# Kernel optimization log

Measured on AMD Instinct MI355X. Metric: run time of the kernel, lower is better.

Reference implementation:

```python
import jax, jax.numpy as jnp
import numpy as np

DEPTH = 6; HEADS = 6; DIM = 384; HD = DIM // HEADS
WS = 14; WINDOW_BLOCKS = (0, 1, 3, 4)
IMG = 512; PATCH = 16; GRID = IMG // PATCH        # 32x32 token grid
PRE_GRID = 14                                      # 224 // 16 pretrain grid
SCALE = HD ** -0.5


def layer_norm(x, w, b, eps=1e-5):
    u = x.mean(-1, keepdims=True)
    s = ((x - u) ** 2).mean(-1, keepdims=True)
    return (x - u) / jnp.sqrt(s + eps) * w + b


def get_rel_pos(size, rel_pos):
    # q_size == k_size here; relative coords in [0, 2*size-2]
    coords = jnp.arange(size)[:, None] - jnp.arange(size)[None, :] + (size - 1)
    return rel_pos[coords]  # (size, size, HD)


def attention(x, qkv_w, qkv_b, proj_w, proj_b, rel_h, rel_w):
    B, H, W, C = x.shape
    N = H * W
    qkv = (x.reshape(B, N, C) @ qkv_w.T + qkv_b).reshape(B, N, 3, HEADS, HD)
    qkv = jnp.moveaxis(qkv, 2, 0).transpose(0, 1, 3, 2, 4)  # (3,B,h,N,d)
    q, k, v = qkv[0], qkv[1], qkv[2]
    attn = jnp.einsum('bhqd,bhkd->bhqk', q * SCALE, k)
    # decomposed relative position bias (ViTDet add_decomposed_rel_pos)
    Rh = get_rel_pos(H, rel_h)  # (H,H,d)
    Rw = get_rel_pos(W, rel_w)  # (W,W,d)
    rq = q.reshape(B, HEADS, H, W, HD)
    bias_h = jnp.einsum('bnhwc,hkc->bnhwk', rq, Rh)  # (B,h,H,W,H)
    bias_w = jnp.einsum('bnhwc,wkc->bnhwk', rq, Rw)  # (B,h,H,W,W)
    attn = (attn.reshape(B, HEADS, H, W, H, W)
            + bias_h[..., :, None] + bias_w[..., None, :]).reshape(B, HEADS, N, N)
    attn = jax.nn.softmax(attn, axis=-1)
    out = jnp.einsum('bhqk,bhkd->bhqd', attn, v)
    out = out.transpose(0, 2, 1, 3).reshape(B, H, W, C)
    return out @ proj_w.T + proj_b


def window_partition(x, ws):
    B, H, W, C = x.shape
    pad_h = (ws - H % ws) % ws
    pad_w = (ws - W % ws) % ws
    x = jnp.pad(x, ((0, 0), (0, pad_h), (0, pad_w), (0, 0)))
    Hp, Wp = H + pad_h, W + pad_w
    x = x.reshape(B, Hp // ws, ws, Wp // ws, ws, C)
    x = x.transpose(0, 1, 3, 2, 4, 5).reshape(-1, ws, ws, C)
    return x, Hp, Wp


def window_unpartition(win, ws, Hp, Wp, H, W):
    B = win.shape[0] // ((Hp // ws) * (Wp // ws))
    x = win.reshape(B, Hp // ws, Wp // ws, ws, ws, -1)
    x = x.transpose(0, 1, 3, 2, 4, 5).reshape(B, Hp, Wp, -1)
    return x[:, :H, :W]


def block(x, p, windowed):
    shortcut = x
    x = layer_norm(x, p['n1w'], p['n1b'])
    if windowed:
        H, W = x.shape[1], x.shape[2]
        x, Hp, Wp = window_partition(x, WS)
    x = attention(x, p['qw'], p['qb'], p['pw'], p['pb'], p['rh'], p['rw'])
    if windowed:
        x = window_unpartition(x, WS, Hp, Wp, H, W)
    x = shortcut + x
    h = layer_norm(x, p['n2w'], p['n2b'])
    h = jax.nn.gelu(h @ p['f1w'].T + p['f1b'], approximate=False)
    return x + h @ p['f2w'].T + p['f2b']


def vit_forward(x, patch_w, patch_b, pos_embed, norm1_w, norm1_b, qkv_w, qkv_b,
                proj_w, proj_b, norm2_w, norm2_b, fc1_w, fc1_b, fc2_w, fc2_b,
                rel_pos_h, rel_pos_w):
    y = jax.lax.conv_general_dilated(
        x, patch_w, (PATCH, PATCH), 'VALID',
        dimension_numbers=('NCHW', 'OIHW', 'NCHW'))
    y = y.transpose(0, 2, 3, 1) + patch_b  # (B, GRID, GRID, DIM)
    # abs pos embed: bicubic resize from pretrain 14x14 grid to 32x32
    pos = pos_embed.reshape(1, PRE_GRID, PRE_GRID, DIM)
    pos = jax.image.resize(pos, (1, GRID, GRID, DIM), 'bicubic')
    y = y + pos
    for i in range(DEPTH):
        windowed = i in WINDOW_BLOCKS
        L = 2 * WS - 1 if windowed else 2 * GRID - 1
        p = dict(n1w=norm1_w[i], n1b=norm1_b[i], qw=qkv_w[i], qb=qkv_b[i],
                 pw=proj_w[i], pb=proj_b[i], rh=rel_pos_h[i, :L], rw=rel_pos_w[i, :L],
                 n2w=norm2_w[i], n2b=norm2_b[i], f1w=fc1_w[i], f1b=fc1_b[i],
                 f2w=fc2_w[i], f2b=fc2_b[i])
        y = block(y, p, windowed)
    return y.transpose(0, 3, 1, 2)  # (B, DIM, GRID, GRID) 'last_feat'


def setup_inputs() -> dict:
    key = jax.random.key(0)
    ks = jax.random.split(key, 10)
    B = 4
    std = 0.02
    f32 = jnp.float32
    return {
        'x': jax.random.normal(ks[0], (B, 3, IMG, IMG), f32),
        'patch_w': jax.random.normal(ks[1], (DIM, 3, PATCH, PATCH), f32) * 0.05,
        'patch_b': jnp.zeros((DIM,), f32),
        'pos_embed': jax.random.normal(ks[2], (1, PRE_GRID * PRE_GRID, DIM), f32) * std,
        'norm1_w': jnp.ones((DEPTH, DIM), f32),
        'norm1_b': jnp.zeros((DEPTH, DIM), f32),
        'qkv_w': jax.random.normal(ks[3], (DEPTH, 3 * DIM, DIM), f32) * std,
        'qkv_b': jnp.zeros((DEPTH, 3 * DIM), f32),
        'proj_w': jax.random.normal(ks[4], (DEPTH, DIM, DIM), f32) * std,
        'proj_b': jnp.zeros((DEPTH, DIM), f32),
        'norm2_w': jnp.ones((DEPTH, DIM), f32),
        'norm2_b': jnp.zeros((DEPTH, DIM), f32),
        'fc1_w': jax.random.normal(ks[5], (DEPTH, 4 * DIM, DIM), f32) * std,
        'fc1_b': jnp.zeros((DEPTH, 4 * DIM), f32),
        'fc2_w': jax.random.normal(ks[6], (DEPTH, DIM, 4 * DIM), f32) * std,
        'fc2_b': jnp.zeros((DEPTH, DIM), f32),
        'rel_pos_h': jax.random.normal(ks[7], (DEPTH, 2 * GRID - 1, HD), f32) * std,
        'rel_pos_w': jax.random.normal(ks[8], (DEPTH, 2 * GRID - 1, HD), f32) * std,
    }


def reference(x, patch_w, patch_b, pos_embed, norm1_w, norm1_b, qkv_w, qkv_b,
              proj_w, proj_b, norm2_w, norm2_b, fc1_w, fc1_b, fc2_w, fc2_b,
              rel_pos_h, rel_pos_w):
    return vit_forward(x, patch_w, patch_b, pos_embed, norm1_w, norm1_b, qkv_w, qkv_b,
                       proj_w, proj_b, norm2_w, norm2_b, fc1_w, fc1_b, fc2_w, fc2_b,
                       rel_pos_h, rel_pos_w)
```

## Files before the change

kernel.cpp:

```cpp
#include <hip/hip_runtime.h>
#include <hip/hip_bf16.h>
#include <math.h>

#define B_SZ 4
#define DIM 384
#define HEADS 6
#define HD 64
#define NTOK 4096
#define WS 14
#define NWIN 36
#define WTOK 196

typedef unsigned short u16;
typedef __bf16 bf16_t;
typedef bf16_t bf16x8 __attribute__((ext_vector_type(8)));
typedef float f32x4 __attribute__((ext_vector_type(4)));

__device__ __forceinline__ float bf2f(unsigned u) { return __uint_as_float(u << 16); }
__device__ __forceinline__ u16 f2bf(float f) {
    unsigned u = __float_as_uint(f);
    unsigned r = (u + 0x7fffu + ((u >> 16) & 1u)) >> 16;
    return (u16)r;
}
__device__ __forceinline__ unsigned pk2bf(float a, float b) {
    __hip_bfloat162 h = __float22bfloat162_rn(make_float2(a, b));
    unsigned r; __builtin_memcpy(&r, &h, 4); return r;
}

__device__ __forceinline__ void ldsload16(const u16* g, u16* l) {
    __builtin_amdgcn_global_load_lds(
        (const __attribute__((address_space(1))) unsigned int*)g,
        (__attribute__((address_space(3))) unsigned int*)l, 16, 0, 0);
}

__device__ __forceinline__ int swz(int r) { return (r ^ (r >> 2)) & 3; }

__device__ __forceinline__ void xcd_remap(int& bx, int& by) {
    int nwg = gridDim.x * gridDim.y;
    int id = blockIdx.y * gridDim.x + blockIdx.x;
    if ((nwg & 7) == 0) {
        int nid = (id & 7) * (nwg >> 3) + (id >> 3);
        by = nid / gridDim.x;
        bx = nid - by * gridDim.x;
    } else {
        bx = blockIdx.x; by = blockIdx.y;
    }
}

__device__ inline float cubic_keys(float x) {
    x = fabsf(x);
    if (x <= 1.f) return ((1.5f * x - 2.5f) * x) * x + 1.f;
    if (x < 2.f)  return ((-0.5f * x + 2.5f) * x - 4.f) * x + 2.f;
    return 0.f;
}

__global__ __launch_bounds__(256) void setup_kernel(
        const float* __restrict__ p0, const float* __restrict__ p1,
        const float* __restrict__ p2, const float* __restrict__ p3,
        const float* __restrict__ p4, const float* __restrict__ p5,
        u16* __restrict__ wb, const float* __restrict__ pe,
        float* __restrict__ posr, const float* __restrict__ x,
        u16* __restrict__ col) {
    int i = (blockIdx.x * 256 + threadIdx.x) * 4;
    if (i < 10918656) {
        const float* s; int off;
        if      (i <   294912) { s = p0; off = 0; }
        else if (i <  2949120) { s = p1; off = 294912; }
        else if (i <  3833856) { s = p2; off = 2949120; }
        else if (i <  7372800) { s = p3; off = 3833856; }
        else if (i < 10911744) { s = p4; off = 7372800; }
        else                   { s = p5; off = 10911744; }
        float4 v = *(const float4*)(s + (i - off));
        u16 o[4] = { f2bf(v.x), f2bf(v.y), f2bf(v.z), f2bf(v.w) };
        *(uint2*)(wb + i) = *(const uint2*)o;
        return;
    }
    i -= 10918656;
    if (i < 393216) {
        int c = i % 384;
        int g = i / 384;
        int gy = g / 32, gx = g % 32;
        float wy[14], wx[14];
        float sy = (gy + 0.5f) * (14.f / 32.f) - 0.5f;
        float sx = (gx + 0.5f) * (14.f / 32.f) - 0.5f;
        float toty = 0.f, totx = 0.f;
        #pragma unroll
        for (int k = 0; k < 14; ++k) {
            wy[k] = cubic_keys(sy - (float)k); toty += wy[k];
            wx[k] = cubic_keys(sx - (float)k); totx += wx[k];
        }
        float4 acc = {0.f, 0.f, 0.f, 0.f};
        #pragma unroll 1
        for (int iy = 0; iy < 14; ++iy) {
            if (wy[iy] == 0.f) continue;
            float4 row = {0.f, 0.f, 0.f, 0.f};
            for (int ix = 0; ix < 14; ++ix) {
                if (wx[ix] == 0.f) continue;
                float4 pv = *(const float4*)(pe + (iy * 14 + ix) * 384 + c);
                row.x += wx[ix] * pv.x; row.y += wx[ix] * pv.y;
                row.z += wx[ix] * pv.z; row.w += wx[ix] * pv.w;
            }
            acc.x += wy[iy] * row.x; acc.y += wy[iy] * row.y;
            acc.z += wy[iy] * row.z; acc.w += wy[iy] * row.w;
        }
        float inv = 1.f / (toty * totx);
        acc.x *= inv; acc.y *= inv; acc.z *= inv; acc.w *= inv;
        *(float4*)(posr + i) = acc;
        return;
    }
    i -= 393216;
    if (i < 3145728) {
        int kk = i % 768;
        int p  = i / 768;
        int b  = p / 1024;
        int ph = (p % 1024) / 32;
        int pw = p % 32;
        int c = kk / 256;
        int r = kk % 256;
        int ii = r / 16, j = r % 16;
        float4 v = *(const float4*)(x + (size_t)b * 3 * 512 * 512 +
                                    (size_t)c * 512 * 512 +
                                    (size_t)(ph * 16 + ii) * 512 + (pw * 16 + j));
        u16 o[4] = { f2bf(v.x), f2bf(v.y), f2bf(v.z), f2bf(v.w) };
        *(uint2*)(col + i) = *(const uint2*)o;
    }
}

__global__ __launch_bounds__(256) void ln_kernel(const float* __restrict__ y,
        const float* __restrict__ lw, const float* __restrict__ lb,
        u16* __restrict__ lnout)
{
    int tok = blockIdx.x * 4 + (threadIdx.x >> 6);
    int t = threadIdx.x & 63;
    size_t base = (size_t)tok * 384;
    float v[6];
    float s = 0.f;
    #pragma unroll
    for (int i = 0; i < 6; ++i) {
        v[i] = y[base + t + 64 * i]; s += v[i];
    }
    #pragma unroll
    for (int off = 32; off > 0; off >>= 1) s += __shfl_xor(s, off);
    float mean = s * (1.f / 384.f);
    float vs = 0.f;
    #pragma unroll
    for (int i = 0; i < 6; ++i) { float d = v[i] - mean; vs += d * d; }
    #pragma unroll
    for (int off = 32; off > 0; off >>= 1) vs += __shfl_xor(vs, off);
    float inv = rsqrtf(vs * (1.f / 384.f) + 1e-5f);
    u16* orow = lnout + base;
    #pragma unroll
    for (int i = 0; i < 6; ++i) {
        int c = t + 64 * i;
        orow[c] = f2bf((v[i] - mean) * inv * lw[c] + lb[c]);
    }
}

__global__ __launch_bounds__(256) void out_transpose(const float* __restrict__ y,
        float* __restrict__ outT)
{
    __shared__ float T[64][65];
    int c0 = blockIdx.x * 64, m0 = blockIdx.y * 64;
    int t = threadIdx.x;
    int cl = t & 63, wv = t >> 6;
    #pragma unroll
    for (int r = 0; r < 16; ++r) {
        int ml = wv * 16 + r;
        T[ml][cl] = y[(size_t)(m0 + ml) * 384 + c0 + cl];
    }
    __syncthreads();
    int b = m0 >> 10, g0 = m0 & 1023;
    int gl = t & 63;
    #pragma unroll
    for (int r = 0; r < 16; ++r) {
        int ccl = wv * 16 + r;
        outT[((size_t)(b * 384 + c0 + ccl)) * 1024 + g0 + gl] = T[gl][ccl];
    }
}

__global__ __launch_bounds__(256) void mfma_gemm4(
        const u16* __restrict__ A, const u16* __restrict__ Wt,
        const float* __restrict__ bias,
        u16* __restrict__ outb,
        int M, int N, int K, int act)
{
    __shared__ u16 As[2][8192];
    __shared__ u16 Bs[2][4096];
    int t = threadIdx.x;
    int lane = t & 63, wave = t >> 6;
    int wm = (wave >> 1) * 64, wn = (wave & 1) * 32;
    int bx, by;
    xcd_remap(bx, by);
    int m0 = by * 128, n0 = bx * 64;

    int r0 = t >> 2,        c0 = ((t & 3) ^ swz(t >> 2)) * 8;
    int r1 = 64 + (t >> 2), c1 = ((t & 3) ^ swz(64 + (t >> 2))) * 8;
    const u16* a0 = A + (size_t)(m0 + r0) * K + c0;
    const u16* a1 = A + (size_t)(m0 + r1) * K + c1;
    const u16* b0 = Wt + (size_t)(n0 + r0) * K + c0;

    auto stage = [&](int k0, int buf) {
        ldsload16(a0 + k0,      &As[buf][wave * 512]);
        ldsload16(a1 + k0,      &As[buf][2048 + wave * 512]);
        ldsload16(b0 + k0,      &Bs[buf][wave * 512]);
        ldsload16(a0 + k0 + 32, &As[buf][4096 + wave * 512]);
        ldsload16(a1 + k0 + 32, &As[buf][6144 + wave * 512]);
        ldsload16(b0 + k0 + 32, &Bs[buf][2048 + wave * 512]);
    };

    f32x4 acc[4][2] = {};
    int row_a = wm + (lane & 15);
    int row_b = wn + (lane & 15);
    int lq = lane >> 4;
    int nchunks = K / 64;

    stage(0, 0);
    __syncthreads();

    for (int ci = 0; ci < nchunks; ++ci) {
        int p = ci & 1;
        bool pref = (ci + 1 < nchunks);
        if (pref) stage((ci + 1) * 64, 1 - p);
        #pragma unroll
        for (int hf = 0; hf < 2; ++hf) {
            bf16x8 af[4], bfr[2];
            #pragma unroll
            for (int i = 0; i < 4; ++i) {
                int r = row_a + i * 16;
                af[i] = *(const bf16x8*)&As[p][hf * 4096 + r * 32 + ((lq ^ swz(r)) * 8)];
            }
            #pragma unroll
            for (int j = 0; j < 2; ++j) {
                int r = row_b + j * 16;
                bfr[j] = *(const bf16x8*)&Bs[p][hf * 2048 + r * 32 + ((lq ^ swz(r)) * 8)];
            }
            #pragma unroll
            for (int i = 0; i < 4; ++i)
                #pragma unroll
                for (int j = 0; j < 2; ++j)
                    acc[i][j] = __builtin_amdgcn_mfma_f32_16x16x32_bf16(
                        af[i], bfr[j], acc[i][j], 0, 0, 0);
        }
        if (pref) __syncthreads();
    }

    int colq = lane & 15, rowq = (lane >> 4) * 4;
    #pragma unroll
    for (int i = 0; i < 4; ++i) {
        #pragma unroll
        for (int rr = 0; rr < 4; ++rr) {
            int m = m0 + wm + i * 16 + rowq + rr;
            size_t mo = (size_t)m * N;
            #pragma unroll
            for (int j = 0; j < 2; ++j) {
                int n = n0 + wn + j * 16 + colq;
                float v = acc[i][j][rr] + bias[n];
                if (act)  v = 0.5f * v * (1.f + erff(v * 0.70710678118654752f));
                outb[mo + n] = f2bf(v);
            }
        }
    }
}

__global__ __launch_bounds__(256) void mfma_gemm64b(
        const u16* __restrict__ A, const u16* __restrict__ Wt,
        const float* __restrict__ bias, u16* __restrict__ outb,
        int M, int N, int K)
{
    __shared__ u16 As[2][4096];
    __shared__ u16 Bs[2][4096];
    int t = threadIdx.x;
    int lane = t & 63, wave = t >> 6;
    int wm = (wave >> 1) * 32, wn = (wave & 1) * 32;
    int bx, by;
    xcd_remap(bx, by);
    int m0 = by * 64, n0 = bx * 64;

    int r0 = t >> 2, c0 = ((t & 3) ^ swz(t >> 2)) * 8;
    const u16* a0 = A + (size_t)(m0 + r0) * K + c0;
    const u16* b0 = Wt + (size_t)(n0 + r0) * K + c0;

    auto stage = [&](int k0, int buf) {
        ldsload16(a0 + k0,      &As[buf][wave * 512]);
        ldsload16(b0 + k0,      &Bs[buf][wave * 512]);
        ldsload16(a0 + k0 + 32, &As[buf][2048 + wave * 512]);
        ldsload16(b0 + k0 + 32, &Bs[buf][2048 + wave * 512]);
    };

    f32x4 acc[2][2] = {};
    int row_a = wm + (lane & 15);
    int row_b = wn + (lane & 15);
    int lq = lane >> 4;
    int nchunks = K / 64;

    stage(0, 0);
    __syncthreads();

    for (int ci = 0; ci < nchunks; ++ci) {
        int p = ci & 1;
        bool pref = (ci + 1 < nchunks);
        if (pref) stage((ci + 1) * 64, 1 - p);
        #pragma unroll
        for (int hf = 0; hf < 2; ++hf) {
            bf16x8 af[2], bfr[2];
            #pragma unroll
            for (int i = 0; i < 2; ++i) {
                int r = row_a + i * 16;
                af[i] = *(const bf16x8*)&As[p][hf * 2048 + r * 32 + ((lq ^ swz(r)) * 8)];
            }
            #pragma unroll
            for (int j = 0; j < 2; ++j) {
                int r = row_b + j * 16;
                bfr[j] = *(const bf16x8*)&Bs[p][hf * 2048 + r * 32 + ((lq ^ swz(r)) * 8)];
            }
            #pragma unroll
            for (int i = 0; i < 2; ++i)
                #pragma unroll
                for (int j = 0; j < 2; ++j)
                    acc[i][j] = __builtin_amdgcn_mfma_f32_16x16x32_bf16(
                        af[i], bfr[j], acc[i][j], 0, 0, 0);
        }
        if (pref) __syncthreads();
    }

    int colq = lane & 15, rowq = (lane >> 4) * 4;
    #pragma unroll
    for (int i = 0; i < 2; ++i) {
        #pragma unroll
        for (int rr = 0; rr < 4; ++rr) {
            int m = m0 + wm + i * 16 + rowq + rr;
            size_t mo = (size_t)m * N;
            #pragma unroll
            for (int j = 0; j < 2; ++j) {
                int n = n0 + wn + j * 16 + colq;
                outb[mo + n] = f2bf(acc[i][j][rr] + bias[n]);
            }
        }
    }
}

__global__ __launch_bounds__(256) void mfma_gemm32(
        const u16* __restrict__ A, const u16* __restrict__ Wt,
        const float* __restrict__ bias, const float* __restrict__ posr,
        float* __restrict__ y, int addy, int M, int N, int K)
{
    __shared__ u16 As[2][8192];
    __shared__ u16 Bs[2][4096];
    int t = threadIdx.x;
    int lane = t & 63, wave = t >> 6;
    int wm = (wave >> 1) * 32, wn = (wave & 1) * 16;
    int bx, by;
    xcd_remap(bx, by);
    int m0 = by * 64, n0 = bx * 32;

    int r0 = t >> 2, c0 = ((t & 3) ^ swz(t >> 2)) * 8;
    const u16* a0 = A + (size_t)(m0 + r0) * K + c0;
    int tb = t & 127;
    int rb = tb >> 2, cb = ((tb & 3) ^ swz(tb >> 2)) * 8;
    const u16* b0 = Wt + (size_t)(n0 + rb) * K + cb;

    auto stage = [&](int k0, int buf) {
        ldsload16(a0 + k0,      &As[buf][wave * 512]);
        ldsload16(a0 + k0 + 32, &As[buf][2048 + wave * 512]);
        ldsload16(a0 + k0 + 64, &As[buf][4096 + wave * 512]);
        ldsload16(a0 + k0 + 96, &As[buf][6144 + wave * 512]);
        if (wave < 2) {
            ldsload16(b0 + k0,      &Bs[buf][wave * 512]);
            ldsload16(b0 + k0 + 64, &Bs[buf][2048 + wave * 512]);
        } else {
            ldsload16(b0 + k0 + 32, &Bs[buf][1024 + (wave - 2) * 512]);
            ldsload16(b0 + k0 + 96, &Bs[buf][3072 + (wave - 2) * 512]);
        }
    };

    f32x4 acc[2] = {};
    int row_a = wm + (lane & 15);
    int row_b = wn + (lane & 15);
    int lq = lane >> 4;
    int nchunks = K / 128;

    stage(0, 0);
    __syncthreads();

    for (int ci = 0; ci < nchunks; ++ci) {
        int p = ci & 1;
        bool pref = (ci + 1 < nchunks);
        if (pref) stage((ci + 1) * 128, 1 - p);
        #pragma unroll
        for (int hf = 0; hf < 4; ++hf) {
            bf16x8 af[2], bf0;
            #pragma unroll
            for (int i = 0; i < 2; ++i) {
                int r = row_a + i * 16;
                af[i] = *(const bf16x8*)&As[p][hf * 2048 + r * 32 + ((lq ^ swz(r)) * 8)];
            }
            {
                int r = row_b;
                bf0 = *(const bf16x8*)&Bs[p][hf * 1024 + r * 32 + ((lq ^ swz(r)) * 8)];
            }
            #pragma unroll
            for (int i = 0; i < 2; ++i)
                acc[i] = __builtin_amdgcn_mfma_f32_16x16x32_bf16(
                    af[i], bf0, acc[i], 0, 0, 0);
        }
        if (pref) __syncthreads();
    }

    int colq = lane & 15, rowq = (lane >> 4) * 4;
    #pragma unroll
    for (int i = 0; i < 2; ++i) {
        #pragma unroll
        for (int rr = 0; rr < 4; ++rr) {
            int m = m0 + wm + i * 16 + rowq + rr;
            size_t mo = (size_t)m * N;
            int n = n0 + wn + colq;
            float v = acc[i][rr] + bias[n];
            if (posr) v += posr[(size_t)(m & 1023) * 384 + n];
            if (addy) v += y[mo + n];
            y[mo + n] = v;
        }
    }
}

template<int N, int W>
__global__ __launch_bounds__(256) void attn_mfma(const u16* __restrict__ qkv,
        const u16* __restrict__ qkb, const float* __restrict__ rh,
        const float* __restrict__ rw, u16* __restrict__ outb,
        float* __restrict__ opart, float* __restrict__ lpart)
{
    constexpr int JS = (W == 32) ? 64 : 32;
    constexpr int L  = (W == 32) ? 63 : 27;
    constexpr int CTR = W - 1;
    constexpr int KSPAN = (W == 32) ? 512 : 224;
    constexpr int NKT = KSPAN / 32;
    __shared__ u16 KV[11776];
    __shared__ u16 bhl[64 * 66];
    __shared__ u16 bwl[64 * 66];
    __shared__ u16 Qt[64 * 66];
    __shared__ unsigned kofs[224];

    u16* Pb = KV + 9216;
    u16* Rt = KV;

    int t = threadIdx.x, lane = t & 63, wave = t >> 6;
    int quad = lane >> 4, l15 = lane & 15;
    int uh = blockIdx.x, qb0 = blockIdx.y * 64;
    int z = (W == 32) ? blockIdx.z : 0;
    int kstart = z * KSPAN;
    int h = uh % HEADS, u = uh / HEADS;
    size_t tbase = (size_t)u * 1024;
    int wb_ = u / 9, wr = u - wb_ * 9;
    int wy = wr / 3, wx = wr - wy * 3;

    auto tok14 = [&](int iy, int ix) -> const u16* {
        int gy = wy * WS + iy, gx = wx * WS + ix;
        if (gy < 32 && gx < 32)
            return qkv + (size_t)(wb_ * 1024 + gy * 32 + gx) * 1152;
        return qkb;
    };
    auto rowptr = [&](int lq2) -> const u16* {
        if constexpr (W == 32) {
            return qkv + (tbase + lq2) * 1152;
        } else {
            int iy = lq2 / WS, ix = lq2 - iy * WS;
            return tok14(iy, ix);
        }
    };

    {
        int q = t & 63, ch0 = (t >> 6) * 16;
        int qc = qb0 + q; if (qc >= N) qc = N - 1;
        const u16* qp = rowptr(qc) + h * 64 + ch0;
        uint4 a = *(const uint4*)qp;
        uint4 b = *(const uint4*)(qp + 8);
        u16 vals[16];
        *(uint4*)vals = a; *(uint4*)(vals + 8) = b;
        #pragma unroll
        for (int c = 0; c < 16; ++c)
            Qt[(ch0 + c) * 66 + q] = ((qb0 + q) < N) ? vals[c] : (u16)0;
    }

    if constexpr (W != 32) {
        if (t < 224) {
            int kh = t / WS;
            kofs[t] = (unsigned)kh | ((unsigned)(t - kh * WS) << 16);
        }
    }

    for (int idx = t; idx < JS * 16; idx += 256) {
        int table = (idx >= JS * 8) ? 1 : 0;
        int id2 = idx & (JS * 8 - 1);
        int j = id2 >> 3, cc0 = (id2 & 7) * 8;
        const float* tab = table ? rw : rh;
        u16 tmp[8];
        if (j < L) {
            const float* src = tab + (size_t)j * 64 + cc0;
            #pragma unroll
            for (int c = 0; c < 8; ++c) tmp[c] = f2bf(src[c]);
        } else {
            #pragma unroll
            for (int c = 0; c < 8; ++c) tmp[c] = 0;
        }
        *(uint4*)&Rt[table * JS * 72 + j * 72 + cc0] = *(uint4*)tmp;
    }
    __syncthreads();

    {
        int tb0 = (W == 32) ? 0 : (wave >> 1);
        int ntb = (W == 32) ? 2 : 1;
        int jt  = (W == 32) ? wave : (wave & 1);
        for (int tt = 0; tt < ntb; ++tt) {
            int table = tb0 + tt;
            const u16* Rtt = Rt + table * JS * 72;
            bf16x8 af0 = *(const bf16x8*)&Rtt[(jt * 16 + l15) * 72 + quad * 8];
            bf16x8 af1 = *(const bf16x8*)&Rtt[(jt * 16 + l15) * 72 + 32 + quad * 8];
            u16* dst = table ? bwl : bhl;
            #pragma unroll
            for (int qt = 0; qt < 4; ++qt) {
                bf16x8 qf0, qf1;
                u16* p0 = (u16*)&qf0; u16* p1 = (u16*)&qf1;
                #pragma unroll
                for (int zz = 0; zz < 8; ++zz) {
                    p0[zz] = Qt[(quad * 8 + zz) * 66 + qt * 16 + l15];
                    p1[zz] = Qt[(32 + quad * 8 + zz) * 66 + qt * 16 + l15];
                }
                f32x4 acc = {};
                acc = __builtin_amdgcn_mfma_f32_16x16x32_bf16(af0, qf0, acc, 0, 0, 0);
                acc = __builtin_amdgcn_mfma_f32_16x16x32_bf16(af1, qf1, acc, 0, 0, 0);
                #pragma unroll
                for (int r = 0; r < 4; ++r)
                    dst[(qt * 16 + l15) * 66 + jt * 16 + quad * 4 + r] = f2bf(acc[r]);
            }
        }
    }
    __syncthreads();

    int skey = (wave * 64 + lane) >> 3;
    int sc8  = ((wave * 64 + lane) & 7) ^ (skey & 7);
    int vkey = t & 31, vch0 = (t >> 5) * 8;
    int siy = 0, six = 0, viy = 0, vix = 0;
    if constexpr (W != 32) {
        int k0 = kstart + skey;
        siy = k0 / WS; six = k0 - siy * WS;
        int k1 = kstart + vkey;
        viy = k1 / WS; vix = k1 - viy * WS;
    }
    auto adv = [](int& iy, int& ix) { ix += 4; iy += 2; if (ix >= WS) { ix -= WS; ++iy; } };

    {
        const u16* kp = (W == 32) ? qkv + (tbase + kstart + skey) * 1152
                                  : tok14(siy, six);
        ldsload16(kp + 384 + h * 64 + sc8 * 8, KV + wave * 512);
        const u16* vp = (W == 32) ? qkv + (tbase + kstart + vkey) * 1152
                                  : tok14(viy, vix);
        uint4 vv = *(const uint4*)(vp + 768 + h * 64 + vch0);
        u16 tmp[8]; *(uint4*)tmp = vv;
        u16* vdst = KV + 4096;
        #pragma unroll
        for (int c = 0; c < 8; ++c) vdst[(vch0 + c) * 40 + vkey] = tmp[c];
        if constexpr (W != 32) { adv(siy, six); adv(viy, vix); }
    }

    bf16x8 qf[2];
    #pragma unroll
    for (int hc = 0; hc < 2; ++hc) {
        u16* qv = (u16*)&qf[hc];
        #pragma unroll
        for (int j = 0; j < 8; ++j)
            qv[j] = Qt[(hc * 32 + quad * 8 + j) * 66 + wave * 16 + l15];
    }
    int qme = wave * 16 + l15;
    bool wactive = (W == 32) ? true : ((qb0 + wave * 16) < N);
    int qq = qb0 + qme; if (qq >= N) qq = N - 1;
    int qh = qq / W, qw = qq - qh * W;
    int qh13 = qh + CTR, qw13 = qw + CTR;
    float bwreg[2][4];
    if constexpr (W == 32) {
        #pragma unroll
        for (int kc2 = 0; kc2 < 2; ++kc2)
            #pragma unroll
            for (int r = 0; r < 4; ++r) {
                int keyl = kc2 * 16 + quad * 4 + r;
                bwreg[kc2][r] = bf2f(bwl[qme * 66 + (qw - keyl + CTR)]);
            }
    }

    f32x4 of[4] = {};
    float lsum = 0.f;
    __syncthreads();

    for (int kt = 0; kt < NKT; ++kt) {
        int kb = kstart + kt * 32;
        int p = kt & 1;
        const u16* ksp = KV + p * 2048;
        const u16* vtp = KV + 4096 + p * 2560;
        bool pref = (kt + 1 < NKT);
        uint4 vpref;
        if (pref) {
            const u16* kp = (W == 32) ? qkv + (tbase + kb + 32 + skey) * 1152
                                      : tok14(siy, six);
            ldsload16(kp + 384 + h * 64 + sc8 * 8, KV + (1 - p) * 2048 + wave * 512);
            const u16* vp = (W == 32) ? qkv + (tbase + kb + 32 + vkey) * 1152
                                      : tok14(viy, vix);
            vpref = *(const uint4*)(vp + 768 + h * 64 + vch0);
            if constexpr (W != 32) { adv(siy, six); adv(viy, vix); }
        }

        if (wactive) {
            f32x4 st[2] = {};
            #pragma unroll
            for (int hc = 0; hc < 2; ++hc) {
                #pragma unroll
                for (int kc2 = 0; kc2 < 2; ++kc2) {
                    int key = kc2 * 16 + l15;
                    int c8 = hc * 4 + quad;
                    int pp = key * 8 + (c8 ^ (key & 7));
                    bf16x8 kf = *(const bf16x8*)&ksp[pp * 8];
                    st[kc2] = __builtin_amdgcn_mfma_f32_16x16x32_bf16(
                        kf, qf[hc], st[kc2], 0, 0, 0);
                }
            }
            float bh_t = 0.f;
            if constexpr (W == 32) bh_t = bf2f(bhl[qme * 66 + (qh - (kb >> 5) + CTR)]);
            #pragma unroll
            for (int kc2 = 0; kc2 < 2; ++kc2) {
                float pv4[4];
                #pragma unroll
                for (int r = 0; r < 4; ++r) {
                    int keyl = kc2 * 16 + quad * 4 + r;
                    float pv;
                    if constexpr (W == 32) {
                        float b = bh_t + bwreg[kc2][r];
                        pv = __expf(fmaf(st[kc2][r], 0.125f, b));
                    } else {
                        unsigned ko = kofs[kb + keyl];
                        float b = bf2f(bhl[qme * 66 + qh13 - (int)(ko & 0xffffu)]) +
                                  bf2f(bwl[qme * 66 + qw13 - (int)(ko >> 16)]);
                        pv = __expf(fmaf(st[kc2][r], 0.125f, b));
                        if (kb + keyl >= N) pv = 0.f;
                    }
                    lsum += pv;
                    pv4[r] = pv;
                }
                uint2 pk;
                pk.x = pk2bf(pv4[0], pv4[1]);
                pk.y = pk2bf(pv4[2], pv4[3]);
                *(uint2*)&Pb[wave * 640 + l15 * 40 + kc2 * 16 + quad * 4] = pk;
            }
            bf16x8 pf = *(const bf16x8*)&Pb[wave * 640 + l15 * 40 + quad * 8];
            #pragma unroll
            for (int ca = 0; ca < 4; ++ca) {
                bf16x8 vf = *(const bf16x8*)&vtp[(ca * 16 + l15) * 40 + quad * 8];
                of[ca] = __builtin_amdgcn_mfma_f32_16x16x32_bf16(
                    vf, pf, of[ca], 0, 0, 0);
            }
        }

        if (pref) {
            u16 tmp[8]; *(uint4*)tmp = vpref;
            u16* vdst = KV + 4096 + (1 - p) * 2560;
            #pragma unroll
            for (int c = 0; c < 8; ++c) vdst[(vch0 + c) * 40 + vkey] = tmp[c];
            __syncthreads();
        }
    }

    lsum += __shfl_xor(lsum, 16);
    lsum += __shfl_xor(lsum, 32);
    int q = qb0 + qme;
    if constexpr (W == 32) {
        size_t ridx = (size_t)z * 24576 + (size_t)uh * 1024 + q;
        float* op = opart + ridx * 64;
        #pragma unroll
        for (int ca = 0; ca < 4; ++ca)
            *(float4*)&op[ca * 16 + quad * 4] = (float4){of[ca][0], of[ca][1],
                                                         of[ca][2], of[ca][3]};
        if (quad == 0) lpart[ridx] = lsum;
    } else {
        float inv = 1.f / lsum;
        if (q < N) {
            int iy = q / WS, ix = q - iy * WS;
            int gy = wy * WS + iy, gx = wx * WS + ix;
            if (gy >= 32 || gx >= 32) return;
            u16* op = outb + (size_t)(wb_ * 1024 + gy * 32 + gx) * 384 + h * 64;
            #pragma unroll
            for (int ca = 0; ca < 4; ++ca) {
                uint2 pk;
                pk.x = pk2bf(of[ca][0] * inv, of[ca][1] * inv);
                pk.y = pk2bf(of[ca][2] * inv, of[ca][3] * inv);
                *(uint2*)&op[ca * 16 + quad * 4] = pk;
            }
        }
    }
}

__global__ __launch_bounds__(256) void attn_merge_kernel(const float* __restrict__ O,
        const float* __restrict__ Lp, u16* __restrict__ attb)
{
    int gi = blockIdx.x * 256 + threadIdx.x;
    int idx = gi >> 4;
    int ch = (gi & 15) * 4;
    float4 o0 = *(const float4*)&O[(size_t)idx * 64 + ch];
    float4 o1 = *(const float4*)&O[((size_t)24576 + idx) * 64 + ch];
    float inv = 1.f / (Lp[idx] + Lp[24576 + idx]);
    int uh = idx >> 10, q = idx & 1023;
    int u = uh / 6, h = uh - u * 6;
    uint2 pk;
    pk.x = pk2bf((o0.x + o1.x) * inv, (o0.y + o1.y) * inv);
    pk.y = pk2bf((o0.z + o1.z) * inv, (o0.w + o1.w) * inv);
    *(uint2*)(attb + ((size_t)(u * 1024 + q)) * 384 + h * 64 + ch) = pk;
}

static inline void launch_gemm(const u16* A, const u16* W, const float* bias,
                               u16* outb, int M, int N, int K, int act,
                               hipStream_t s) {
    dim3 g(N / 64, M / 128, 1);
    mfma_gemm4<<<g, 256, 0, s>>>(A, W, bias, outb, M, N, K, act);
}

static inline void launch_gemm64b(const u16* A, const u16* W, const float* bias,
                                  u16* outb, int M, int N, int K, hipStream_t s) {
    dim3 g(N / 64, M / 64, 1);
    mfma_gemm64b<<<g, 256, 0, s>>>(A, W, bias, outb, M, N, K);
}

static inline void launch_gemm32(const u16* A, const u16* W, const float* bias,
                                 const float* posr, float* y, int addy,
                                 int M, int N, int K, hipStream_t s) {
    dim3 g(N / 32, M / 64, 1);
    mfma_gemm32<<<g, 256, 0, s>>>(A, W, bias, posr, y, addy, M, N, K);
}

extern "C" void kernel_launch(void* const* d_in, const int* in_sizes, int n_in,
                              void* d_out, int out_size, void* d_ws, size_t ws_size,
                              hipStream_t stream) {
    const float* x      = (const float*)d_in[0];
    const float* patchw = (const float*)d_in[1];
    const float* patchb = (const float*)d_in[2];
    const float* pos    = (const float*)d_in[3];
    const float* n1w    = (const float*)d_in[4];
    const float* n1b    = (const float*)d_in[5];
    const float* qkvw   = (const float*)d_in[6];
    const float* qkvb   = (const float*)d_in[7];
    const float* pw     = (const float*)d_in[8];
    const float* pb     = (const float*)d_in[9];
    const float* n2w    = (const float*)d_in[10];
    const float* n2b    = (const float*)d_in[11];
    const float* f1w    = (const float*)d_in[12];
    const float* f1b    = (const float*)d_in[13];
    const float* f2w    = (const float*)d_in[14];
    const float* f2b    = (const float*)d_in[15];
    const float* rph    = (const float*)d_in[16];
    const float* rpw    = (const float*)d_in[17];
    float* out = (float*)d_out;

    float* y   = (float*)d_ws;
    u16* attb  = (u16*)(y + 1572864);
    u16* mlpb  = attb + 1572864;
    u16* lnb   = mlpb + 6291456;
    u16* qkvx  = lnb + 1572864;
    u16* rsrv  = qkvx + 4718592;
    u16* wb    = rsrv + 7864320;
    float* posr = (float*)(wb + 10918656);

    u16* colb  = rsrv;
    float* Opart   = (float*)mlpb;
    float* Lpart   = (float*)lnb;

    u16* wb_patch = wb;
    u16* wb_qkv   = wb + 294912;
    u16* wb_pw    = wb + 2949120;
    u16* wb_f1    = wb + 3833856;
    u16* wb_f2    = wb + 7372800;
    u16* wqb      = wb + 10911744;

    setup_kernel<<<(14457600 / 4 + 255) / 256, 256, 0, stream>>>(
        patchw, qkvw, pw, f1w, f2w, qkvb, wb, pos, posr, x, colb);

    launch_gemm32(colb, wb_patch, patchb, posr, y, 0, NTOK, 384, 768, stream);
    ln_kernel<<<1024, 256, 0, stream>>>(y, n1w, n1b, lnb);

    for (int i = 0; i < 6; ++i) {
        bool windowed = (i == 0 || i == 1 || i == 3 || i == 4);
        const float* rh = rph + (size_t)i * 63 * 64;
        const float* rw = rpw + (size_t)i * 63 * 64;
        launch_gemm64b(lnb, wb_qkv + (size_t)i * 442368, qkvb + i * 1152,
                       qkvx, NTOK, 1152, 384, stream);
        if (windowed) {
            attn_mfma<WTOK, WS><<<dim3(NWIN * HEADS, 4, 1), 256, 0, stream>>>(
                qkvx, wqb + i * 1152, rh, rw, attb, nullptr, nullptr);
        } else {
            attn_mfma<1024, 32><<<dim3(B_SZ * HEADS, 16, 2), 256, 0, stream>>>(
                qkvx, wqb + i * 1152, rh, rw, nullptr, Opart, Lpart);
            attn_merge_kernel<<<1536, 256, 0, stream>>>(Opart, Lpart, attb);
        }
        launch_gemm32(attb, wb_pw + (size_t)i * 147456, pb + i * 384,
                      nullptr, y, 1, NTOK, 384, 384, stream);
        ln_kernel<<<1024, 256, 0, stream>>>(y, n2w + i * 384, n2b + i * 384, lnb);
        launch_gemm(lnb, wb_f1 + (size_t)i * 589824, f1b + i * 1536,
                    mlpb, NTOK, 1536, 384, 1, stream);
        launch_gemm32(mlpb, wb_f2 + (size_t)i * 589824, f2b + i * 384,
                      nullptr, y, 1, NTOK, 384, 1536, stream);
        if (i < 5)
            ln_kernel<<<1024, 256, 0, stream>>>(y, n1w + (i + 1) * 384,
                                                n1b + (i + 1) * 384, lnb);
        else
            out_transpose<<<dim3(6, 64), 256, 0, stream>>>(y, out);
    }
}
```

Before: 641.9 us.

## Fuse LayerNorm into residual GEMM epilogue via last-block-per-row-tile counter

Removes the standalone LayerNorm kernels. Each residual-writing GEMM now increments a per-row-tile atomic counter, and the last block to finish a 64-row tile computes LayerNorm for those rows and writes the bf16 output. This saves 13 kernel launches and one extra global read pass scheduled separately. In exchange, the LayerNorm for each tile runs serially in a single block at the tail of the GEMM, and correctness depends on threadfence ordering and on the counters being reset.

```diff
diff --git a/kernel.cpp b/kernel.cpp
--- a/kernel.cpp
+++ b/kernel.cpp
@@ -60,8 +60,10 @@
         const float* __restrict__ p4, const float* __restrict__ p5,
         u16* __restrict__ wb, const float* __restrict__ pe,
         float* __restrict__ posr, const float* __restrict__ x,
-        u16* __restrict__ col) {
-    int i = (blockIdx.x * 256 + threadIdx.x) * 4;
+        u16* __restrict__ col, int* __restrict__ cnt) {
+    int raw = blockIdx.x * 256 + threadIdx.x;
+    if (raw < 64) cnt[raw] = 0;
+    int i = raw * 4;
     if (i < 10918656) {
         const float* s; int off;
         if      (i <   294912) { s = p0; off = 0; }
@@ -126,36 +128,6 @@
     }
 }
 
-__global__ __launch_bounds__(256) void ln_kernel(const float* __restrict__ y,
-        const float* __restrict__ lw, const float* __restrict__ lb,
-        u16* __restrict__ lnout)
-{
-    int tok = blockIdx.x * 4 + (threadIdx.x >> 6);
-    int t = threadIdx.x & 63;
-    size_t base = (size_t)tok * 384;
-    float v[6];
-    float s = 0.f;
-    #pragma unroll
-    for (int i = 0; i < 6; ++i) {
-        v[i] = y[base + t + 64 * i]; s += v[i];
-    }
-    #pragma unroll
-    for (int off = 32; off > 0; off >>= 1) s += __shfl_xor(s, off);
-    float mean = s * (1.f / 384.f);
-    float vs = 0.f;
-    #pragma unroll
-    for (int i = 0; i < 6; ++i) { float d = v[i] - mean; vs += d * d; }
-    #pragma unroll
-    for (int off = 32; off > 0; off >>= 1) vs += __shfl_xor(vs, off);
-    float inv = rsqrtf(vs * (1.f / 384.f) + 1e-5f);
-    u16* orow = lnout + base;
-    #pragma unroll
-    for (int i = 0; i < 6; ++i) {
-        int c = t + 64 * i;
-        orow[c] = f2bf((v[i] - mean) * inv * lw[c] + lb[c]);
-    }
-}
-
 __global__ __launch_bounds__(256) void out_transpose(const float* __restrict__ y,
         float* __restrict__ outT)
 {
@@ -342,7 +314,9 @@
 __global__ __launch_bounds__(256) void mfma_gemm32(
         const u16* __restrict__ A, const u16* __restrict__ Wt,
         const float* __restrict__ bias, const float* __restrict__ posr,
-        float* __restrict__ y, int addy, int M, int N, int K)
+        float* __restrict__ y, int addy, int M, int N, int K,
+        const float* __restrict__ lw, const float* __restrict__ lb,
+        u16* __restrict__ lnout, int* __restrict__ cnt)
 {
     __shared__ u16 As[2][8192];
     __shared__ u16 Bs[2][4096];
@@ -418,6 +392,44 @@
             if (posr) v += posr[(size_t)(m & 1023) * 384 + n];
             if (addy) v += y[mo + n];
             y[mo + n] = v;
+        }
+    }
+
+    if (lnout) {
+        __shared__ int tick;
+        __threadfence();
+        __syncthreads();
+        if (t == 0) tick = atomicAdd(&cnt[by], 1);
+        __syncthreads();
+        if (tick == (int)gridDim.x - 1) {
+            __threadfence();
+            int wv = t >> 6, ln = t & 63;
+            for (int rr = 0; rr < 16; ++rr) {
+                int row = m0 + wv * 16 + rr;
+                size_t base = (size_t)row * 384;
+                float v[6];
+                float s = 0.f;
+                #pragma unroll
+                for (int i = 0; i < 6; ++i) {
+                    v[i] = y[base + ln + 64 * i]; s += v[i];
+                }
+                #pragma unroll
+                for (int off = 32; off > 0; off >>= 1) s += __shfl_xor(s, off);
+                float mean = s * (1.f / 384.f);
+                float vs = 0.f;
+                #pragma unroll
+                for (int i = 0; i < 6; ++i) { float d = v[i] - mean; vs += d * d; }
+                #pragma unroll
+                for (int off = 32; off > 0; off >>= 1) vs += __shfl_xor(vs, off);
+                float inv = rsqrtf(vs * (1.f / 384.f) + 1e-5f);
+                u16* orow = lnout + base;
+                #pragma unroll
+                for (int i = 0; i < 6; ++i) {
+                    int c = ln + 64 * i;
+                    orow[c] = f2bf((v[i] - mean) * inv * lw[c] + lb[c]);
+                }
+            }
+            if (t == 0) cnt[by] = 0;
         }
     }
 }
@@ -726,9 +738,12 @@
 
 static inline void launch_gemm32(const u16* A, const u16* W, const float* bias,
                                  const float* posr, float* y, int addy,
-                                 int M, int N, int K, hipStream_t s) {
+                                 int M, int N, int K,
+                                 const float* lw, const float* lb, u16* lnout,
+                                 int* cnt, hipStream_t s) {
     dim3 g(N / 32, M / 64, 1);
-    mfma_gemm32<<<g, 256, 0, s>>>(A, W, bias, posr, y, addy, M, N, K);
+    mfma_gemm32<<<g, 256, 0, s>>>(A, W, bias, posr, y, addy, M, N, K,
+                                  lw, lb, lnout, cnt);
 }
 
 extern "C" void kernel_launch(void* const* d_in, const int* in_sizes, int n_in,
@@ -762,6 +777,7 @@
     u16* rsrv  = qkvx + 4718592;
     u16* wb    = rsrv + 7864320;
     float* posr = (float*)(wb + 10918656);
+    int* cnt   = (int*)(posr + 393216);
 
     u16* colb  = rsrv;
     float* Opart   = (float*)mlpb;
@@ -775,10 +791,10 @@
     u16* wqb      = wb + 10911744;
 
     setup_kernel<<<(14457600 / 4 + 255) / 256, 256, 0, stream>>>(
-        patchw, qkvw, pw, f1w, f2w, qkvb, wb, pos, posr, x, colb);
-
-    launch_gemm32(colb, wb_patch, patchb, posr, y, 0, NTOK, 384, 768, stream);
-    ln_kernel<<<1024, 256, 0, stream>>>(y, n1w, n1b, lnb);
+        patchw, qkvw, pw, f1w, f2w, qkvb, wb, pos, posr, x, colb, cnt);
+
+    launch_gemm32(colb, wb_patch, patchb, posr, y, 0, NTOK, 384, 768,
+                  n1w, n1b, lnb, cnt, stream);
 
     for (int i = 0; i < 6; ++i) {
         bool windowed = (i == 0 || i == 1 || i == 3 || i == 4);
@@ -795,16 +811,20 @@
             attn_merge_kernel<<<1536, 256, 0, stream>>>(Opart, Lpart, attb);
         }
         launch_gemm32(attb, wb_pw + (size_t)i * 147456, pb + i * 384,
-                      nullptr, y, 1, NTOK, 384, 384, stream);
-        ln_kernel<<<1024, 256, 0, stream>>>(y, n2w + i * 384, n2b + i * 384, lnb);
+                      nullptr, y, 1, NTOK, 384, 384,
+                      n2w + i * 384, n2b + i * 384, lnb, cnt, stream);
         launch_gemm(lnb, wb_f1 + (size_t)i * 589824, f1b + i * 1536,
                     mlpb, NTOK, 1536, 384, 1, stream);
-        launch_gemm32(mlpb, wb_f2 + (size_t)i * 589824, f2b + i * 384,
-                      nullptr, y, 1, NTOK, 384, 1536, stream);
         if (i < 5)
-            ln_kernel<<<1024, 256, 0, stream>>>(y, n1w + (i + 1) * 384,
-                                                n1b + (i + 1) * 384, lnb);
-        else
+            launch_gemm32(mlpb, wb_f2 + (size_t)i * 589824, f2b + i * 384,
+                          nullptr, y, 1, NTOK, 384, 1536,
+                          n1w + (i + 1) * 384, n1b + (i + 1) * 384, lnb, cnt,
+                          stream);
+        else {
+            launch_gemm32(mlpb, wb_f2 + (size_t)i * 589824, f2b + i * 384,
+                          nullptr, y, 1, NTOK, 384, 1536,
+                          nullptr, nullptr, nullptr, cnt, stream);
             out_transpose<<<dim3(6, 64), 256, 0, stream>>>(y, out);
-    }
-}
+        }
+    }
+}
```

New measurement: 1.568 ms. +144.2%, slower.

## Fuse norm1 LayerNorm into QKV GEMM by folding affine params into weights

Applied to the files above, without the earlier changes.

Removes the separate norm1 LayerNorm kernels. The LN gain is folded into the bf16 QKV weights and the LN bias into a precomputed QKV bias during setup. The QKV GEMM now reads fp32 residual rows directly, computes per-row mean and rstd in a prologue, and normalizes while staging A tiles into shared memory. In exchange, every N-tile block recomputes row statistics and reads fp32 A (twice the bytes), with synchronous staging instead of async LDS loads.

```diff
diff --git a/kernel.cpp b/kernel.cpp
--- a/kernel.cpp
+++ b/kernel.cpp
@@ -60,7 +60,8 @@
         const float* __restrict__ p4, const float* __restrict__ p5,
         u16* __restrict__ wb, const float* __restrict__ pe,
         float* __restrict__ posr, const float* __restrict__ x,
-        u16* __restrict__ col) {
+        u16* __restrict__ col, const float* __restrict__ n1w_,
+        const float* __restrict__ n1b_, float* __restrict__ qb2) {
     int i = (blockIdx.x * 256 + threadIdx.x) * 4;
     if (i < 10918656) {
         const float* s; int off;
@@ -71,6 +72,13 @@
         else if (i < 10911744) { s = p4; off = 7372800; }
         else                   { s = p5; off = 10911744; }
         float4 v = *(const float4*)(s + (i - off));
+        if (s == p1) {
+            int j = i - 294912;
+            int layer = j / 442368;
+            int c = j % 384;
+            const float* lwp = n1w_ + layer * 384 + c;
+            v.x *= lwp[0]; v.y *= lwp[1]; v.z *= lwp[2]; v.w *= lwp[3];
+        }
         u16 o[4] = { f2bf(v.x), f2bf(v.y), f2bf(v.z), f2bf(v.w) };
         *(uint2*)(wb + i) = *(const uint2*)o;
         return;
@@ -123,6 +131,18 @@
                                     (size_t)(ph * 16 + ii) * 512 + (pw * 16 + j));
         u16 o[4] = { f2bf(v.x), f2bf(v.y), f2bf(v.z), f2bf(v.w) };
         *(uint2*)(col + i) = *(const uint2*)o;
+        return;
+    }
+    i -= 3145728;
+    if (i < 27648) {
+        int o = i >> 2;
+        int l = o / 1152, n = o - l * 1152;
+        const float* wrow = p1 + (size_t)(l * 1152 + n) * 384;
+        const float* lbp = n1b_ + l * 384;
+        float s2 = p5[l * 1152 + n];
+        #pragma unroll 4
+        for (int c = 0; c < 384; ++c) s2 += lbp[c] * wrow[c];
+        qb2[o] = s2;
     }
 }
 
@@ -262,13 +282,14 @@
     }
 }
 
-__global__ __launch_bounds__(256) void mfma_gemm64b(
-        const u16* __restrict__ A, const u16* __restrict__ Wt,
+__global__ __launch_bounds__(256) void mfma_gemm64ln(
+        const float* __restrict__ yA, const u16* __restrict__ Wt,
         const float* __restrict__ bias, u16* __restrict__ outb,
         int M, int N, int K)
 {
-    __shared__ u16 As[2][4096];
+    __shared__ __align__(16) u16 As[2][4096];
     __shared__ u16 Bs[2][4096];
+    __shared__ float sstat[64][2];
     int t = threadIdx.x;
     int lane = t & 63, wave = t >> 6;
     int wm = (wave >> 1) * 32, wn = (wave & 1) * 32;
@@ -277,14 +298,45 @@
     int m0 = by * 64, n0 = bx * 64;
 
     int r0 = t >> 2, c0 = ((t & 3) ^ swz(t >> 2)) * 8;
-    const u16* a0 = A + (size_t)(m0 + r0) * K + c0;
+    const float* a0f = yA + (size_t)(m0 + r0) * 384 + c0;
     const u16* b0 = Wt + (size_t)(n0 + r0) * K + c0;
 
+    for (int i = 0; i < 16; ++i) {
+        int row = wave * 16 + i;
+        const float* yr = yA + (size_t)(m0 + row) * 384;
+        float v[6]; float s = 0.f;
+        #pragma unroll
+        for (int j = 0; j < 6; ++j) { v[j] = yr[lane + 64 * j]; s += v[j]; }
+        #pragma unroll
+        for (int off = 32; off > 0; off >>= 1) s += __shfl_xor(s, off);
+        float mean = s * (1.f / 384.f);
+        float vs = 0.f;
+        #pragma unroll
+        for (int j = 0; j < 6; ++j) { float d = v[j] - mean; vs += d * d; }
+        #pragma unroll
+        for (int off = 32; off > 0; off >>= 1) vs += __shfl_xor(vs, off);
+        if (lane == 0) {
+            sstat[row][0] = mean;
+            sstat[row][1] = rsqrtf(vs * (1.f / 384.f) + 1e-5f);
+        }
+    }
+    __syncthreads();
+    float meanr = sstat[r0][0], rstdr = sstat[r0][1];
+
     auto stage = [&](int k0, int buf) {
-        ldsload16(a0 + k0,      &As[buf][wave * 512]);
         ldsload16(b0 + k0,      &Bs[buf][wave * 512]);
-        ldsload16(a0 + k0 + 32, &As[buf][2048 + wave * 512]);
         ldsload16(b0 + k0 + 32, &Bs[buf][2048 + wave * 512]);
+        #pragma unroll
+        for (int hh = 0; hh < 2; ++hh) {
+            float4 f0 = *(const float4*)(a0f + k0 + hh * 32);
+            float4 f1 = *(const float4*)(a0f + k0 + hh * 32 + 4);
+            u16 o[8] = {
+                f2bf((f0.x - meanr) * rstdr), f2bf((f0.y - meanr) * rstdr),
+                f2bf((f0.z - meanr) * rstdr), f2bf((f0.w - meanr) * rstdr),
+                f2bf((f1.x - meanr) * rstdr), f2bf((f1.y - meanr) * rstdr),
+                f2bf((f1.z - meanr) * rstdr), f2bf((f1.w - meanr) * rstdr) };
+            *(uint4*)&As[buf][hh * 2048 + t * 8] = *(const uint4*)o;
+        }
     };
 
     f32x4 acc[2][2] = {};
@@ -718,10 +770,11 @@
     mfma_gemm4<<<g, 256, 0, s>>>(A, W, bias, outb, M, N, K, act);
 }
 
-static inline void launch_gemm64b(const u16* A, const u16* W, const float* bias,
-                                  u16* outb, int M, int N, int K, hipStream_t s) {
+static inline void launch_gemm64ln(const float* yA, const u16* W,
+                                   const float* bias, u16* outb,
+                                   int M, int N, int K, hipStream_t s) {
     dim3 g(N / 64, M / 64, 1);
-    mfma_gemm64b<<<g, 256, 0, s>>>(A, W, bias, outb, M, N, K);
+    mfma_gemm64ln<<<g, 256, 0, s>>>(yA, W, bias, outb, M, N, K);
 }
 
 static inline void launch_gemm32(const u16* A, const u16* W, const float* bias,
@@ -762,6 +815,7 @@
     u16* rsrv  = qkvx + 4718592;
     u16* wb    = rsrv + 7864320;
     float* posr = (float*)(wb + 10918656);
+    float* qb2  = posr + 393216;
 
     u16* colb  = rsrv;
     float* Opart   = (float*)mlpb;
@@ -774,18 +828,18 @@
     u16* wb_f2    = wb + 7372800;
     u16* wqb      = wb + 10911744;
 
-    setup_kernel<<<(14457600 / 4 + 255) / 256, 256, 0, stream>>>(
-        patchw, qkvw, pw, f1w, f2w, qkvb, wb, pos, posr, x, colb);
+    setup_kernel<<<(14485248 / 4 + 255) / 256, 256, 0, stream>>>(
+        patchw, qkvw, pw, f1w, f2w, qkvb, wb, pos, posr, x, colb,
+        n1w, n1b, qb2);
 
     launch_gemm32(colb, wb_patch, patchb, posr, y, 0, NTOK, 384, 768, stream);
-    ln_kernel<<<1024, 256, 0, stream>>>(y, n1w, n1b, lnb);
 
     for (int i = 0; i < 6; ++i) {
         bool windowed = (i == 0 || i == 1 || i == 3 || i == 4);
         const float* rh = rph + (size_t)i * 63 * 64;
         const float* rw = rpw + (size_t)i * 63 * 64;
-        launch_gemm64b(lnb, wb_qkv + (size_t)i * 442368, qkvb + i * 1152,
-                       qkvx, NTOK, 1152, 384, stream);
+        launch_gemm64ln(y, wb_qkv + (size_t)i * 442368, qb2 + i * 1152,
+                        qkvx, NTOK, 1152, 384, stream);
         if (windowed) {
             attn_mfma<WTOK, WS><<<dim3(NWIN * HEADS, 4, 1), 256, 0, stream>>>(
                 qkvx, wqb + i * 1152, rh, rw, attb, nullptr, nullptr);
@@ -801,10 +855,7 @@
                     mlpb, NTOK, 1536, 384, 1, stream);
         launch_gemm32(mlpb, wb_f2 + (size_t)i * 589824, f2b + i * 384,
                       nullptr, y, 1, NTOK, 384, 1536, stream);
-        if (i < 5)
-            ln_kernel<<<1024, 256, 0, stream>>>(y, n1w + (i + 1) * 384,
-                                                n1b + (i + 1) * 384, lnb);
-        else
+        if (i == 5)
             out_transpose<<<dim3(6, 64), 256, 0, stream>>>(y, out);
     }
 }
```

Measured after the change: 757.5 us. 1.18x slower.
